# Optimization experiments

Measured on AMD Instinct MI355X. Metric: run time of the kernel, lower is better.

Reference implementation:

```python
import jax, jax.numpy as jnp
import numpy as np

C = 10  # cluster gap window; repo-level global constant in the original code


def _per_neuron(v, label):
    """Faithful vectorized translation of the per-(batch,neuron) Python loops.

    v:     [T] membrane potential trace
    label: scalar int target cluster count
    Returns (loss_contribution, num_cluster).
    """
    T = v.shape[0]
    t = jnp.arange(T, dtype=jnp.int32)
    spk = v >= 0.0                                   # spike positions (v >= 0)
    # exclusive prefix counts of spikes: csp[i] = #spikes in v[:i]
    csp = jnp.concatenate([jnp.zeros(1, jnp.int32), jnp.cumsum(spk.astype(jnp.int32))])
    lo = jnp.clip(t - C, 0, T)
    # a spike starts a new cluster iff no spike in the preceding C steps
    cnt_prev = csp[t] - csp[lo]
    is_start = spk & (cnt_prev == 0)
    num_cluster = jnp.sum(is_start.astype(jnp.int32))
    vmax = jnp.max(v)

    # ---- excess branch (label > num_cluster) ----
    # mask[t] = 1 iff some spike lies in [t-C, t+C]  (union of [first-C, last+C] per cluster)
    hi = jnp.clip(t + C + 1, 0, T)
    mask = (csp[hi] - csp[lo]) > 0
    full0 = jnp.all(mask)
    NEG = jnp.asarray(-1e30, v.dtype)
    m0 = jnp.max(jnp.where(mask, NEG, v))            # max over unmasked times (iter 0)
    tm = jnp.argmax(v)                               # original uses global argmax of v
    win = (t >= tm - C // 2) & (t <= tm + C // 2)
    mask2 = mask | win                               # mask after first loop iteration (fixed thereafter)
    full2 = jnp.all(mask2)
    # if mask2 full, remaining iterations pick a spike value (random in original; spikes have v>=0,
    # we use the deterministic surrogate vmax which is always a spike value when spikes exist)
    m_rest = jnp.where(full2, vmax, jnp.max(jnp.where(mask2, NEG, v)))
    label_f = label.astype(v.dtype)
    ncf = num_cluster.astype(v.dtype)
    dE = jnp.maximum(label_f - ncf, 1.0)             # safe denominator (branch-gated below)
    mean_excess = (m0 + (dE - 1.0) * m_rest) / dE
    excess_loss = jnp.where(full0, vmax, -mean_excess)

    # ---- deficit branch (label < num_cluster) ----
    BIG = T + 2 * C + 2
    lt = jax.lax.cummax(jnp.where(spk, t, -BIG))                 # nearest spike <= t
    rt = jax.lax.cummin(jnp.where(spk, t, BIG)[::-1])[::-1]      # nearest spike >= t
    in_span = (rt - lt) <= C                                     # t inside [first,last] of a cluster
    cid = jnp.cumsum(is_start.astype(jnp.int32)) - 1             # cluster id at time t
    K = T // (C + 1) + 1                                         # max possible clusters
    seg = jnp.where(in_span, cid, K)
    rec = jax.ops.segment_max(v, seg, num_segments=K + 1)[:K]    # per-cluster span max
    POS = jnp.asarray(1e30, v.dtype)
    rec = jnp.where(jnp.arange(K) < num_cluster, rec, POS)
    rec = jnp.sort(rec)                                          # ascending, real clusters first
    dD = jnp.maximum(ncf - label_f, 1.0)
    deficit_loss = jnp.sum(jnp.where(jnp.arange(K) < (num_cluster - label), rec, 0.0)) / dD

    contrib = jnp.where(label > num_cluster, excess_loss,
                        jnp.where(label < num_cluster, deficit_loss, 0.0))
    return contrib, num_cluster


def setup_inputs() -> dict:
    key = jax.random.key(0)
    k1, k2, k3 = jax.random.split(key, 3)
    B, T, N = 256, 500, 128
    vmem = jax.random.normal(k1, (B, T, N), dtype=jnp.float32)
    vlastmem = jax.random.normal(k2, (B, T, N), dtype=jnp.float32)
    labels_t = jax.random.randint(k3, (B, N), 0, 5, dtype=jnp.int32)
    return {"vmem": vmem, "vlastmem": vlastmem, "labels_t": labels_t, "ratio": 1}


def reference(vmem, vlastmem, labels_t, ratio):
    # vlastmem and ratio are unused in the original forward; kept for signature fidelity.
    vv = jnp.transpose(vmem, (0, 2, 1))  # [B, N, T]
    contrib, nclus = jax.vmap(jax.vmap(_per_neuron))(vv, labels_t)
    loss = jnp.sum(contrib)
    spike_output = nclus.astype(jnp.float32)  # [B, N] cluster counts
    return loss, spike_output
```

## Files before the change

kernel.cpp:

```cpp
#include <hip/hip_runtime.h>

namespace {
constexpr int CC    = 10;
constexpr int TT    = 500;
constexpr int NN    = 128;
constexpr int NG    = 4;
constexpr int LSEG  = TT / NG;
constexpr int HALO  = CC;
constexpr int NCH   = 15;
constexpr int MAXK  = 12;
constexpr int MAXG  = TT / (CC + 1) + 1;
}

__global__ __launch_bounds__(512, 2)
void fused_kernel(const float* __restrict__ vmem, const int* __restrict__ labels,
                  float* __restrict__ out) {
    const int tid = threadIdx.x;
    const int g   = tid >> 7;
    const int n   = tid & 127;
    const int b   = blockIdx.x;
    const int a   = g * LSEG;
    const bool firstSeg = (g == 0), lastSeg = (g == NG - 1);
    const float* __restrict__ col = vmem + (size_t)b * TT * NN + n;

    __shared__ float s_cl[NG][MAXK][NN];
    __shared__ int   s_pk[NG][NN];
    __shared__ float s_hdm[NG][NN], s_tg[NG][NN], s_vm[NG][NN], s_m0[NG][NN];
    __shared__ float s_gl[MAXG][NN];
    __shared__ float wb[2][512];
    __shared__ float red[2];

    float b0[10], b1[10], b2[10], b3[10] = {};

    auto load = [&](float (&d)[10], int c) {
        if ((firstSeg && c == 0) || (lastSeg && c >= 13)) {
            #pragma unroll
            for (int j = 0; j < 10; ++j) {
                int t = a - HALO + 10 * c + j;
                t = t < 0 ? 0 : (t > TT - 1 ? TT - 1 : t);
                d[j] = col[t * NN];
            }
        } else {
            const float* __restrict__ p = col + (a - HALO + 10 * c) * NN;
            #pragma unroll
            for (int j = 0; j < 10; ++j) d[j] = p[j * NN];
        }
    };

    int   ls = -(1 << 20), lcount = 0, hdne = 0, tmn = 0, hasu = 0;
    float ccm = -1e30f, rmax = -1e30f, hdm = -1e30f, vmx = -1e30f, m0 = -1e30f;

    auto scan = [&](const float (&cur)[10], const float (&prev)[10], int c) {
        #pragma unroll
        for (int j = 0; j < 10; ++j) {
            const int ofs = -HALO + 10 * c + j;
            const int t   = a + ofs;
            float v = cur[j];
            if ((ofs < 0 && firstSeg) || (ofs >= LSEG && lastSeg)) v = -1.0f;
            const bool spike = v >= 0.0f;
            if (ofs >= 0 && ofs < LSEG) {
                const float rm2 = fmaxf(rmax, v);
                if (spike) {
                    if (t - ls > CC) {
                        if (lcount > 0) s_cl[g][lcount - 1][n] = ccm;
                        ccm = v; ++lcount;
                    } else if (lcount == 0) { hdne = 1; hdm = fmaxf(hdm, rm2); }
                    else ccm = fmaxf(ccm, rm2);
                    rmax = -1e30f;
                } else rmax = rm2;
                if (v > vmx) { vmx = v; tmn = t; }
            }
            if (spike) ls = t;
            if (ofs >= HALO && ofs < LSEG + HALO) {
                const float vu = prev[j];
                if (ls < t - 2 * CC) { hasu = 1; if (vu > m0) m0 = vu; }
            }
        }
    };

    #define SB __builtin_amdgcn_sched_barrier(0)
    load(b0, 0);  load(b1, 1);  SB;
    load(b2, 2);  SB; scan(b0, b3, 0);  SB;
    load(b3, 3);  SB; scan(b1, b0, 1);  SB;
    load(b0, 4);  SB; scan(b2, b1, 2);  SB;
    load(b1, 5);  SB; scan(b3, b2, 3);  SB;
    load(b2, 6);  SB; scan(b0, b3, 4);  SB;
    load(b3, 7);  SB; scan(b1, b0, 5);  SB;
    load(b0, 8);  SB; scan(b2, b1, 6);  SB;
    load(b1, 9);  SB; scan(b3, b2, 7);  SB;
    load(b2, 10); SB; scan(b0, b3, 8);  SB;
    load(b3, 11); SB; scan(b1, b0, 9);  SB;
    load(b0, 12); SB; scan(b2, b1, 10); SB;
    load(b1, 13); SB; scan(b3, b2, 11); SB;
    load(b2, 14); SB; scan(b0, b3, 12); SB;
    scan(b1, b0, 13); scan(b2, b1, 14);
    #undef SB

    if (lcount > 0) s_cl[g][lcount - 1][n] = ccm;

    s_pk[g][n]  = lcount | (hdne << 4) | (hasu << 5) | (tmn << 6);
    s_hdm[g][n] = hdm;
    s_tg[g][n]  = rmax;
    s_vm[g][n]  = vmx;
    s_m0[g][n]  = m0;
    __syncthreads();

    if (tid < NN) {
        const int lane = tid & 63, wv = tid >> 6;
        int gi = 0, g_nc = 0, g_hasu = 0, g_tm = 0;
        bool open = false; float cur = -1e30f, ptg = -1e30f;
        float g_vmax = -1e30f, g_m0 = -1e30f;
        #pragma unroll
        for (int s = 0; s < NG; ++s) {
            const int pk = s_pk[s][tid];
            const int k = pk & 15, hne = (pk >> 4) & 1;
            g_nc += k; g_hasu |= (pk >> 5) & 1;
            const float vmS = s_vm[s][tid];
            if (vmS > g_vmax) { g_vmax = vmS; g_tm = pk >> 6; }
            const float m0S = s_m0[s][tid];
            if (m0S > g_m0) g_m0 = m0S;
            if (open) {
                if (hne) { cur = fmaxf(cur, fmaxf(ptg, s_hdm[s][tid])); ptg = s_tg[s][tid]; }
                if (k > 0 || !hne) { s_gl[gi][tid] = cur; ++gi; open = false; }
            }
            if (k > 0) {
                for (int i = 0; i < k - 1; ++i) { s_gl[gi][tid] = s_cl[s][i][tid]; ++gi; }
                cur = s_cl[s][k - 1][tid]; open = true; ptg = s_tg[s][tid];
            }
        }
        if (open) { s_gl[gi][tid] = cur; ++gi; }

        const int label = labels[b * NN + tid];

        const bool need2 = (label > g_nc) && g_hasu && (label - g_nc >= 2);
        float mrest = g_vmax;
        unsigned long long bal = __ballot(need2);
        const float* colbase = vmem + (size_t)b * TT * NN;
        float* __restrict__ wbp = wb[wv];
        while (bal) {
            const int fl = __ffsll((unsigned long long)bal) - 1;
            bal &= bal - 1;
            const int   nf    = (wv << 6) | fl;
            const int   tmf   = __shfl(g_tm, fl);
            const float vmaxf = __shfl(g_vmax, fl);
            #pragma unroll
            for (int j = 0; j < 8; ++j) {
                const int t = lane * 8 + j;
                wbp[t] = (t < TT) ? colbase[(size_t)t * NN + nf] : -1.0f;
            }
            asm volatile("s_waitcnt lgkmcnt(0)" ::: "memory");
            __builtin_amdgcn_wave_barrier();
            int ls2 = -1000, lh = 0; float lm = -1e30f;
            const int u0 = lane * 8;
            for (int t2 = u0 - 10; t2 < u0 + 18; ++t2) {
                const float v = (t2 >= 0 && t2 < 512) ? wbp[t2] : -1.0f;
                if (v >= 0.0f) ls2 = t2;
                const int u = t2 - 10;
                if (u >= u0 && u < u0 + 8 && u < TT) {
                    if (ls2 < u - 10 && (u < tmf - CC / 2 || u > tmf + CC / 2)) {
                        lh = 1; const float vu = wbp[u]; if (vu > lm) lm = vu;
                    }
                }
            }
            #pragma unroll
            for (int off = 32; off > 0; off >>= 1) {
                lm = fmaxf(lm, __shfl_down(lm, off));
                lh |= __shfl_down(lh, off);
            }
            const float res = __shfl(lh ? lm : vmaxf, 0);
            if (lane == fl) mrest = res;
            __builtin_amdgcn_wave_barrier();
        }

        float contrib = 0.0f;
        if (label > g_nc) {
            if (!g_hasu) contrib = g_vmax;
            else {
                const float dE = (float)(label - g_nc);
                contrib = -((g_m0 + (dE - 1.0f) * mrest) / dE);
            }
        } else if (label < g_nc) {
            const int kk = g_nc - label;
            float ssum = 0.0f;
            for (int i = 0; i < kk; ++i) {
                float mn = 1e30f; int mj = 0;
                for (int jj = 0; jj < g_nc; ++jj) {
                    const float x = s_gl[jj][tid];
                    if (x < mn) { mn = x; mj = jj; }
                }
                ssum += mn; s_gl[mj][tid] = 1e30f;
            }
            contrib = ssum / (float)kk;
        }

        out[1 + b * NN + tid] = (float)g_nc;

        float w = contrib;
        #pragma unroll
        for (int off = 32; off > 0; off >>= 1) w += __shfl_down(w, off);
        if (lane == 0) red[wv] = w;
    }
    __syncthreads();
    if (tid == 0) atomicAdd(out, red[0] + red[1]);
}

extern "C" void kernel_launch(void* const* d_in, const int* in_sizes, int n_in,
                              void* d_out, int out_size, void* d_ws, size_t ws_size,
                              hipStream_t stream) {
    const float* vmem   = (const float*)d_in[0];
    const int*   labels = (const int*)d_in[2];
    float*       out    = (float*)d_out;
    (void)d_ws; (void)ws_size;

    const int B = in_sizes[2] / NN;

    hipMemsetAsync(out, 0, sizeof(float), stream);
    hipLaunchKernelGGL(fused_kernel, dim3(B), dim3(512), 0, stream, vmem, labels, out);
}
```

Measured before the change: 160.4 us.

## Split time into ten segments and tile neurons 32 per block

Each thread now scans a 50-step time segment instead of a 125-step one, which shortens the serial scan per thread. Blocks handle 32 neurons instead of 128, on a 2D grid of (neuron tiles × batch), so the launch has four times as many blocks and more parallelism and occupancy. Per-segment summaries are packed into one shared record array, and the block-level reduction becomes one atomic per block. The cost is more halo re-reads, narrower 128-byte coalesced accesses, more atomics on the output, and a longer serial merge over ten segments.

```diff
diff --git a/kernel.cpp b/kernel.cpp
--- a/kernel.cpp
+++ b/kernel.cpp
@@ -1,42 +1,39 @@
 #include <hip/hip_runtime.h>
 
 namespace {
-constexpr int CC    = 10;
-constexpr int TT    = 500;
-constexpr int NN    = 128;
-constexpr int NG    = 4;
-constexpr int LSEG  = TT / NG;
-constexpr int HALO  = CC;
-constexpr int NCH   = 15;
-constexpr int MAXK  = 12;
-constexpr int MAXG  = TT / (CC + 1) + 1;
+constexpr int CC   = 10;
+constexpr int TT   = 500;
+constexpr int NN   = 128;
+constexpr int G    = 10;
+constexpr int LSEG = TT / G;
+constexpr int HALO = CC;
+constexpr int NB   = 32;
+constexpr int MAXG = TT / (CC + 1) + 1;
 }
 
-__global__ __launch_bounds__(512, 2)
+__global__ __launch_bounds__(320, 5)
 void fused_kernel(const float* __restrict__ vmem, const int* __restrict__ labels,
                   float* __restrict__ out) {
     const int tid = threadIdx.x;
-    const int g   = tid >> 7;
-    const int n   = tid & 127;
-    const int b   = blockIdx.x;
+    const int g   = tid >> 5;
+    const int ln  = tid & 31;
+    const int b   = blockIdx.y;
+    const int n   = (blockIdx.x << 5) | ln;
     const int a   = g * LSEG;
-    const bool firstSeg = (g == 0), lastSeg = (g == NG - 1);
+    const bool firstSeg = (g == 0), lastSeg = (g == G - 1);
     const float* __restrict__ col = vmem + (size_t)b * TT * NN + n;
 
-    __shared__ float s_cl[NG][MAXK][NN];
-    __shared__ int   s_pk[NG][NN];
-    __shared__ float s_hdm[NG][NN], s_tg[NG][NN], s_vm[NG][NN], s_m0[NG][NN];
-    __shared__ float s_gl[MAXG][NN];
-    __shared__ float wb[2][512];
-    __shared__ float red[2];
+    __shared__ float s_rec[G][10][NB];
+    __shared__ float s_gl[MAXG][NB];
+    __shared__ float wb[512];
 
     float b0[10], b1[10], b2[10], b3[10] = {};
 
     auto load = [&](float (&d)[10], int c) {
-        if ((firstSeg && c == 0) || (lastSeg && c >= 13)) {
+        if ((firstSeg && c == 0) || (lastSeg && c == 6)) {
             #pragma unroll
             for (int j = 0; j < 10; ++j) {
-                int t = a - HALO + 10 * c + j;
+                int t = a + (-HALO + 10 * c + j);
                 t = t < 0 ? 0 : (t > TT - 1 ? TT - 1 : t);
                 d[j] = col[t * NN];
             }
@@ -62,7 +59,7 @@
                 const float rm2 = fmaxf(rmax, v);
                 if (spike) {
                     if (t - ls > CC) {
-                        if (lcount > 0) s_cl[g][lcount - 1][n] = ccm;
+                        if (lcount > 0) s_rec[g][lcount - 1][ln] = ccm;
                         ccm = v; ++lcount;
                     } else if (lcount == 0) { hdne = 1; hdm = fmaxf(hdm, rm2); }
                     else ccm = fmaxf(ccm, rm2);
@@ -71,7 +68,7 @@
                 if (v > vmx) { vmx = v; tmn = t; }
             }
             if (spike) ls = t;
-            if (ofs >= HALO && ofs < LSEG + HALO) {
+            if (ofs >= HALO) {
                 const float vu = prev[j];
                 if (ls < t - 2 * CC) { hasu = 1; if (vu > m0) m0 = vu; }
             }
@@ -79,96 +76,87 @@
     };
 
     #define SB __builtin_amdgcn_sched_barrier(0)
-    load(b0, 0);  load(b1, 1);  SB;
-    load(b2, 2);  SB; scan(b0, b3, 0);  SB;
-    load(b3, 3);  SB; scan(b1, b0, 1);  SB;
-    load(b0, 4);  SB; scan(b2, b1, 2);  SB;
-    load(b1, 5);  SB; scan(b3, b2, 3);  SB;
-    load(b2, 6);  SB; scan(b0, b3, 4);  SB;
-    load(b3, 7);  SB; scan(b1, b0, 5);  SB;
-    load(b0, 8);  SB; scan(b2, b1, 6);  SB;
-    load(b1, 9);  SB; scan(b3, b2, 7);  SB;
-    load(b2, 10); SB; scan(b0, b3, 8);  SB;
-    load(b3, 11); SB; scan(b1, b0, 9);  SB;
-    load(b0, 12); SB; scan(b2, b1, 10); SB;
-    load(b1, 13); SB; scan(b3, b2, 11); SB;
-    load(b2, 14); SB; scan(b0, b3, 12); SB;
-    scan(b1, b0, 13); scan(b2, b1, 14);
+    load(b0, 0); load(b1, 1); SB;
+    load(b2, 2); SB; scan(b0, b3, 0); SB;
+    load(b3, 3); SB; scan(b1, b0, 1); SB;
+    load(b0, 4); SB; scan(b2, b1, 2); SB;
+    load(b1, 5); SB; scan(b3, b2, 3); SB;
+    load(b2, 6); SB; scan(b0, b3, 4); SB;
+    scan(b1, b0, 5); scan(b2, b1, 6);
     #undef SB
 
-    if (lcount > 0) s_cl[g][lcount - 1][n] = ccm;
-
-    s_pk[g][n]  = lcount | (hdne << 4) | (hasu << 5) | (tmn << 6);
-    s_hdm[g][n] = hdm;
-    s_tg[g][n]  = rmax;
-    s_vm[g][n]  = vmx;
-    s_m0[g][n]  = m0;
+    if (lcount > 0) s_rec[g][lcount - 1][ln] = ccm;
+
+    s_rec[g][5][ln] = __int_as_float(lcount | (hdne << 3) | (hasu << 4) | (tmn << 5));
+    s_rec[g][6][ln] = hdm;
+    s_rec[g][7][ln] = rmax;
+    s_rec[g][8][ln] = vmx;
+    s_rec[g][9][ln] = m0;
     __syncthreads();
 
-    if (tid < NN) {
-        const int lane = tid & 63, wv = tid >> 6;
+    if (tid < NB) {
         int gi = 0, g_nc = 0, g_hasu = 0, g_tm = 0;
         bool open = false; float cur = -1e30f, ptg = -1e30f;
         float g_vmax = -1e30f, g_m0 = -1e30f;
         #pragma unroll
-        for (int s = 0; s < NG; ++s) {
-            const int pk = s_pk[s][tid];
-            const int k = pk & 15, hne = (pk >> 4) & 1;
-            g_nc += k; g_hasu |= (pk >> 5) & 1;
-            const float vmS = s_vm[s][tid];
-            if (vmS > g_vmax) { g_vmax = vmS; g_tm = pk >> 6; }
-            const float m0S = s_m0[s][tid];
+        for (int s2 = 0; s2 < G; ++s2) {
+            const int pk = __float_as_int(s_rec[s2][5][tid]);
+            const int k = pk & 7, hne = (pk >> 3) & 1;
+            g_nc += k; g_hasu |= (pk >> 4) & 1;
+            const float vmS = s_rec[s2][8][tid];
+            if (vmS > g_vmax) { g_vmax = vmS; g_tm = pk >> 5; }
+            const float m0S = s_rec[s2][9][tid];
             if (m0S > g_m0) g_m0 = m0S;
             if (open) {
-                if (hne) { cur = fmaxf(cur, fmaxf(ptg, s_hdm[s][tid])); ptg = s_tg[s][tid]; }
+                if (hne) { cur = fmaxf(cur, fmaxf(ptg, s_rec[s2][6][tid]));
+                           ptg = s_rec[s2][7][tid]; }
                 if (k > 0 || !hne) { s_gl[gi][tid] = cur; ++gi; open = false; }
             }
             if (k > 0) {
-                for (int i = 0; i < k - 1; ++i) { s_gl[gi][tid] = s_cl[s][i][tid]; ++gi; }
-                cur = s_cl[s][k - 1][tid]; open = true; ptg = s_tg[s][tid];
+                for (int i = 0; i < k - 1; ++i) { s_gl[gi][tid] = s_rec[s2][i][tid]; ++gi; }
+                cur = s_rec[s2][k - 1][tid]; open = true; ptg = s_rec[s2][7][tid];
             }
         }
         if (open) { s_gl[gi][tid] = cur; ++gi; }
 
-        const int label = labels[b * NN + tid];
+        const int label = labels[b * NN + n];
 
         const bool need2 = (label > g_nc) && g_hasu && (label - g_nc >= 2);
         float mrest = g_vmax;
         unsigned long long bal = __ballot(need2);
         const float* colbase = vmem + (size_t)b * TT * NN;
-        float* __restrict__ wbp = wb[wv];
         while (bal) {
-            const int fl = __ffsll((unsigned long long)bal) - 1;
+            const int fl = __ffsll(bal) - 1;
             bal &= bal - 1;
-            const int   nf    = (wv << 6) | fl;
+            const int   nf    = (blockIdx.x << 5) | fl;
             const int   tmf   = __shfl(g_tm, fl);
             const float vmaxf = __shfl(g_vmax, fl);
             #pragma unroll
-            for (int j = 0; j < 8; ++j) {
-                const int t = lane * 8 + j;
-                wbp[t] = (t < TT) ? colbase[(size_t)t * NN + nf] : -1.0f;
+            for (int j = 0; j < 16; ++j) {
+                const int t = tid * 16 + j;
+                wb[t] = (t < TT) ? colbase[(size_t)t * NN + nf] : -1.0f;
             }
             asm volatile("s_waitcnt lgkmcnt(0)" ::: "memory");
             __builtin_amdgcn_wave_barrier();
             int ls2 = -1000, lh = 0; float lm = -1e30f;
-            const int u0 = lane * 8;
-            for (int t2 = u0 - 10; t2 < u0 + 18; ++t2) {
-                const float v = (t2 >= 0 && t2 < 512) ? wbp[t2] : -1.0f;
+            const int u0 = tid * 16;
+            for (int t2 = u0 - 10; t2 < u0 + 26; ++t2) {
+                const float v = (t2 >= 0 && t2 < 512) ? wb[t2] : -1.0f;
                 if (v >= 0.0f) ls2 = t2;
                 const int u = t2 - 10;
-                if (u >= u0 && u < u0 + 8 && u < TT) {
+                if (u >= u0 && u < u0 + 16 && u < TT) {
                     if (ls2 < u - 10 && (u < tmf - CC / 2 || u > tmf + CC / 2)) {
-                        lh = 1; const float vu = wbp[u]; if (vu > lm) lm = vu;
+                        lh = 1; const float vu = wb[u]; if (vu > lm) lm = vu;
                     }
                 }
             }
             #pragma unroll
-            for (int off = 32; off > 0; off >>= 1) {
+            for (int off = 16; off > 0; off >>= 1) {
                 lm = fmaxf(lm, __shfl_down(lm, off));
                 lh |= __shfl_down(lh, off);
             }
             const float res = __shfl(lh ? lm : vmaxf, 0);
-            if (lane == fl) mrest = res;
+            if (tid == fl) mrest = res;
             __builtin_amdgcn_wave_barrier();
         }
 
@@ -193,15 +181,13 @@
             contrib = ssum / (float)kk;
         }
 
-        out[1 + b * NN + tid] = (float)g_nc;
+        out[1 + b * NN + n] = (float)g_nc;
 
         float w = contrib;
         #pragma unroll
-        for (int off = 32; off > 0; off >>= 1) w += __shfl_down(w, off);
-        if (lane == 0) red[wv] = w;
+        for (int off = 16; off > 0; off >>= 1) w += __shfl_down(w, off);
+        if (tid == 0) atomicAdd(out, w);
     }
-    __syncthreads();
-    if (tid == 0) atomicAdd(out, red[0] + red[1]);
 }
 
 extern "C" void kernel_launch(void* const* d_in, const int* in_sizes, int n_in,
@@ -215,5 +201,6 @@
     const int B = in_sizes[2] / NN;
 
     hipMemsetAsync(out, 0, sizeof(float), stream);
-    hipLaunchKernelGGL(fused_kernel, dim3(B), dim3(512), 0, stream, vmem, labels, out);
+    hipLaunchKernelGGL(fused_kernel, dim3(NN / NB, B), dim3(G * NB), 0, stream,
+                       vmem, labels, out);
 }
```

After: 167.3 us. 1.04x slower.
